# Kernel tuning notes

Measured on AMD Instinct MI355X. Metric: run time of the kernel, lower is better.

## Reference

```python
import jax, jax.numpy as jnp
import numpy as np

D_MODEL = 1024
N_HEADS = 16
D_K = D_MODEL // N_HEADS
EPS = 1e-8


def _l2_rownorm(x):
    # RowNormActivation: normalize each row (last dim) to unit L2 norm
    return x * jax.lax.rsqrt(jnp.sum(x * x, axis=-1, keepdims=True) + EPS)


def setup_inputs() -> dict:
    key = jax.random.key(0)
    ks = jax.random.split(key, 11)
    B, S = 2, 2048
    sc = 1.0 / np.sqrt(D_MODEL)
    inp = {
        "Q": jax.random.normal(ks[0], (B, S, D_MODEL), jnp.float32),
        "K": jax.random.normal(ks[1], (B, S, D_MODEL), jnp.float32),
        "V": jax.random.normal(ks[2], (B, S, D_MODEL), jnp.float32),
        "Wq_w": jax.random.normal(ks[3], (D_MODEL, D_MODEL), jnp.float32) * sc,
        "Wq_b": jnp.zeros((D_MODEL,), jnp.float32),
        "Wk_w": jax.random.normal(ks[4], (D_MODEL, D_MODEL), jnp.float32) * sc,
        "Wk_b": jnp.zeros((D_MODEL,), jnp.float32),
        "Wv_w": jax.random.normal(ks[5], (D_MODEL, D_MODEL), jnp.float32) * sc,
        "Wv_b": jnp.zeros((D_MODEL,), jnp.float32),
        "Wo_w": jax.random.normal(ks[6], (D_MODEL, D_MODEL), jnp.float32) * sc,
        "Wo_b": jnp.zeros((D_MODEL,), jnp.float32),
    }
    return inp


def reference(Q, K, V, Wq_w, Wq_b, Wk_w, Wk_b, Wv_w, Wv_b, Wo_w, Wo_b):
    B, S, _ = Q.shape
    # torch Linear: y = x @ W.T + b
    q = (Q @ Wq_w.T + Wq_b).reshape(B, S, N_HEADS, D_K).transpose(0, 2, 1, 3)
    k = (K @ Wk_w.T + Wk_b).reshape(B, S, N_HEADS, D_K).transpose(0, 2, 1, 3)
    v = (V @ Wv_w.T + Wv_b).reshape(B, S, N_HEADS, D_K).transpose(0, 2, 1, 3)
    qn = _l2_rownorm(q)
    kn = _l2_rownorm(k)
    scores = jnp.einsum("bhqd,bhkd->bhqk", qn, kn)
    attn = scores * scores  # squared similarity, no softmax (dropout=0 / eval)
    out = jnp.einsum("bhqk,bhkd->bhqd", attn, v)
    out = out.transpose(0, 2, 1, 3).reshape(B, S, D_MODEL)
    return out @ Wo_w.T + Wo_b
```

## Files before the change

kernel.cpp:

```cpp
#include <hip/hip_runtime.h>
#include <hip/hip_bf16.h>


#define D_MODEL 1024
#define N_HEADS 16
#define D_K     64
#define BATCH   2
#define SEQ     2048
#define M_TOT   (BATCH * SEQ)

typedef short  s16x8 __attribute__((ext_vector_type(8)));
typedef float  f32x4 __attribute__((ext_vector_type(4)));
typedef unsigned short ushort_t;
typedef ushort_t us4 __attribute__((ext_vector_type(4)));

__device__ __forceinline__ ushort_t f2bf(float f) {
    union { float f; unsigned int u; } x; x.f = f;
    unsigned int u = x.u;
    return (ushort_t)((u + 0x7fffu + ((u >> 16) & 1u)) >> 16);
}
__device__ __forceinline__ float bf2f(ushort_t h) {
    union { unsigned int u; float f; } x; x.u = ((unsigned int)h) << 16;
    return x.f;
}
__device__ __forceinline__ unsigned int pack2bf(float a, float b) {
    union { __hip_bfloat162 h; unsigned int u; } x;
    x.h = __float22bfloat162_rn(float2{a, b});
    return x.u;
}

__device__ __forceinline__ void gload_lds16(const ushort_t* g, ushort_t* l) {
    __builtin_amdgcn_global_load_lds(
        (__attribute__((address_space(1))) void*)(ushort_t*)g,
        (__attribute__((address_space(3))) void*)l, 16, 0, 0);
}

#define WAIT_VM(n)  asm volatile("s_waitcnt vmcnt(" #n ")" ::: "memory")
#define WAIT_LGKM0  asm volatile("s_waitcnt lgkmcnt(0)" ::: "memory")
#define BARRIER     asm volatile("s_barrier" ::: "memory")

struct ConvArgs {
    const float* src[11];
    ushort_t*    dst[11];
    int          n[11];
};

__global__ __launch_bounds__(256) void convert_kernel(ConvArgs a) {
    const int t = blockIdx.y;
    const int i = (blockIdx.x * 256 + threadIdx.x) * 4;
    if (i >= a.n[t]) return;
    const float4 v = *(const float4*)(a.src[t] + i);
    us4 p;
    p[0] = f2bf(v.x); p[1] = f2bf(v.y); p[2] = f2bf(v.z); p[3] = f2bf(v.w);
    *(us4*)(a.dst[t] + i) = p;
}

template <int BM, int MODE>
__device__ __forceinline__ void gemm_body(
    ushort_t* __restrict__ smem,
    const ushort_t* __restrict__ A,
    const ushort_t* __restrict__ W,
    const ushort_t* __restrict__ bias,
    ushort_t* __restrict__ out,
    float* __restrict__ outf,
    int bx, int by)
{
    static_assert(BM == 64 || BM == 128, "");
    constexpr int K    = 1024;
    constexpr int MF   = BM / 32;
    constexpr int BUFW = (BM + 128) * 64;
    constexpr int NIT  = K / 64;

    const int t    = threadIdx.x;
    const int wave = t >> 6;
    const int lane = t & 63;
    const int quad = lane >> 4;
    const int lc   = lane & 15;
    const int wm   = wave >> 1;
    const int wn   = wave & 1;
    const int m0   = bx * BM;
    const int n0   = by * 128;

    f32x4 acc[MF][4];
    const f32x4 zero = {0.f, 0.f, 0.f, 0.f};
#pragma unroll
    for (int i = 0; i < MF; ++i)
#pragma unroll
        for (int j = 0; j < 4; ++j) acc[i][j] = zero;

    auto stage = [&](int buf, int k0) {
        ushort_t* Ast = smem + buf * BUFW;
        ushort_t* Bst = Ast + BM * 64;
#pragma unroll
        for (int c = 0; c < MF; ++c) {
            int idx = c * 256 + t;
            int row = idx >> 3, phys = idx & 7;
            int col = (phys ^ (row & 7)) * 8;
            gload_lds16(A + (size_t)(m0 + row) * K + k0 + col, Ast + idx * 8);
        }
#pragma unroll
        for (int c = 0; c < 4; ++c) {
            int idx = c * 256 + t;
            int row = idx >> 3, phys = idx & 7;
            int col = (phys ^ (row & 7)) * 8;
            gload_lds16(W + (size_t)(n0 + row) * K + k0 + col, Bst + idx * 8);
        }
    };
    auto comp = [&](int buf) {
        ushort_t* Ast = smem + buf * BUFW;
        ushort_t* Bst = Ast + BM * 64;
#pragma unroll
        for (int ks = 0; ks < 2; ++ks) {
            const int ph = ((ks * 4 + quad) ^ (lc & 7)) * 8;
            s16x8 a[MF], b[4];
#pragma unroll
            for (int i = 0; i < MF; ++i)
                a[i] = *(const s16x8*)(Ast + (wm * (BM / 2) + i * 16 + lc) * 64 + ph);
#pragma unroll
            for (int i = 0; i < 4; ++i)
                b[i] = *(const s16x8*)(Bst + (wn * 64 + i * 16 + lc) * 64 + ph);
#pragma unroll
            for (int mf = 0; mf < MF; ++mf)
#pragma unroll
                for (int nf = 0; nf < 4; ++nf)
                    acc[mf][nf] = __builtin_amdgcn_mfma_f32_16x16x32_bf16(
                        a[mf], b[nf], acc[mf][nf], 0, 0, 0);
        }
    };

    stage(0, 0);
    stage(1, 64);
    for (int it = 0; it < NIT - 2; ++it) {
        if constexpr (BM == 128) WAIT_VM(8); else WAIT_VM(6);
        BARRIER;
        comp(it & 1);
        WAIT_LGKM0;
        BARRIER;
        stage(it & 1, (it + 2) * 64);
    }
    if constexpr (BM == 128) WAIT_VM(8); else WAIT_VM(6);
    BARRIER;
    comp((NIT - 2) & 1);
    WAIT_VM(0);
    BARRIER;
    comp((NIT - 1) & 1);

    float bv[4];
#pragma unroll
    for (int nf = 0; nf < 4; ++nf) bv[nf] = bf2f(bias[n0 + wn * 64 + nf * 16 + lc]);

    if (MODE == 0) {
#pragma unroll
        for (int mf = 0; mf < MF; ++mf)
#pragma unroll
            for (int nf = 0; nf < 4; ++nf)
#pragma unroll
                for (int r = 0; r < 4; ++r) {
                    int mg = m0 + wm * (BM / 2) + mf * 16 + quad * 4 + r;
                    int ng = n0 + wn * 64 + nf * 16 + lc;
                    outf[(size_t)mg * D_MODEL + ng] = acc[mf][nf][r] + bv[nf];
                }
    } else if (MODE == 1) {
#pragma unroll
        for (int mf = 0; mf < MF; ++mf)
#pragma unroll
            for (int r = 0; r < 4; ++r) {
                float ss = 0.f;
#pragma unroll
                for (int nf = 0; nf < 4; ++nf) {
                    float v = acc[mf][nf][r] + bv[nf];
                    acc[mf][nf][r] = v;
                    ss += v * v;
                }
                ss += __shfl_xor(ss, 1);
                ss += __shfl_xor(ss, 2);
                ss += __shfl_xor(ss, 4);
                ss += __shfl_xor(ss, 8);
                float inv = rsqrtf(ss + 1e-8f);
                int mg = m0 + wm * (BM / 2) + mf * 16 + quad * 4 + r;
                int b  = mg >> 11;
                int s  = mg & 2047;
#pragma unroll
                for (int nf = 0; nf < 4; ++nf) {
                    int ng = n0 + wn * 64 + nf * 16 + lc;
                    int h = ng >> 6, d = ng & 63;
                    out[(((size_t)(b * N_HEADS + h)) * SEQ + s) * D_K + d] =
                        f2bf(acc[mf][nf][r] * inv);
                }
            }
    } else {
        __syncthreads();
        ushort_t* vt = smem + wave * (64 * 72);
#pragma unroll
        for (int mf = 0; mf < 4; ++mf)
#pragma unroll
            for (int nf = 0; nf < 4; ++nf) {
                us4 p;
#pragma unroll
                for (int r = 0; r < 4; ++r) p[r] = f2bf(acc[mf][nf][r] + bv[nf]);
                *(us4*)(vt + (nf * 16 + lc) * 72 + mf * 16 + quad * 4) = p;
            }
        WAIT_LGKM0;
#pragma unroll
        for (int r = 0; r < 8; ++r) {
            int d  = r * 8 + (lane >> 3);
            int so = (lane & 7) * 8;
            uint4 val = *(const uint4*)(vt + d * 72 + so);
            int mg = m0 + wm * 64 + so;
            int b  = mg >> 11;
            int s  = mg & 2047;
            int ng = n0 + wn * 64 + d;
            int h = ng >> 6, dh = ng & 63;
            *(uint4*)(out + (((size_t)(b * N_HEADS + h)) * D_K + dh) * SEQ + s) = val;
        }
    }
}

__global__ __launch_bounds__(256) void qkv_kernel(
    const ushort_t* __restrict__ Qb, const ushort_t* __restrict__ Kb,
    const ushort_t* __restrict__ Vb,
    const ushort_t* __restrict__ Wq, const ushort_t* __restrict__ Wk,
    const ushort_t* __restrict__ Wv,
    const ushort_t* __restrict__ bq, const ushort_t* __restrict__ bk,
    const ushort_t* __restrict__ bv,
    ushort_t* __restrict__ qn, ushort_t* __restrict__ kn,
    ushort_t* __restrict__ vT)
{
    __shared__ __align__(16) ushort_t smem[2 * (128 + 128) * 64];
    const int z = blockIdx.z;
    if (z == 0)
        gemm_body<128, 1>(smem, Qb, Wq, bq, qn, nullptr, blockIdx.x, blockIdx.y);
    else if (z == 1)
        gemm_body<128, 1>(smem, Kb, Wk, bk, kn, nullptr, blockIdx.x, blockIdx.y);
    else
        gemm_body<128, 2>(smem, Vb, Wv, bv, vT, nullptr, blockIdx.x, blockIdx.y);
}

__global__ __launch_bounds__(256) void wo_kernel(
    const ushort_t* __restrict__ A, const ushort_t* __restrict__ W,
    const ushort_t* __restrict__ bias, float* __restrict__ outf)
{
    __shared__ __align__(16) ushort_t smem[2 * (64 + 128) * 64];
    gemm_body<64, 0>(smem, A, W, bias, nullptr, outf, blockIdx.x, blockIdx.y);
}

__global__ __launch_bounds__(256) void attn_kernel(
    const ushort_t* __restrict__ qn,
    const ushort_t* __restrict__ kn,
    const ushort_t* __restrict__ vT,
    ushort_t* __restrict__ attn_out)
{
    __shared__ __align__(16) ushort_t smem[2 * 8192];
    __shared__ __align__(16) ushort_t Pl[128 * 64];

    const int t    = threadIdx.x;
    const int wave = t >> 6;
    const int lane = t & 63;
    const int quad = lane >> 4;
    const int lc   = lane & 15;
    const int bh   = blockIdx.x;
    const int qt   = blockIdx.y;
    const int b    = bh >> 4;
    const int h    = bh & 15;

    const ushort_t* qb = qn + (size_t)bh * SEQ * D_K;
    const ushort_t* kb = kn + (size_t)bh * SEQ * D_K;
    const ushort_t* vb = vT + (size_t)bh * D_K * SEQ;
    const int q0 = qt * 128;

    s16x8 qf[8][2];
#pragma unroll
    for (int mf = 0; mf < 8; ++mf)
#pragma unroll
        for (int ks = 0; ks < 2; ++ks)
            qf[mf][ks] = *(const s16x8*)(qb + (size_t)(q0 + mf * 16 + lc) * D_K +
                                         ks * 32 + quad * 8);

    f32x4 oacc[2][4];
    const f32x4 zero = {0.f, 0.f, 0.f, 0.f};
#pragma unroll
    for (int mf = 0; mf < 2; ++mf)
#pragma unroll
        for (int df = 0; df < 4; ++df) oacc[mf][df] = zero;

    auto stage = [&](int buf, int j0) {
        ushort_t* kst = smem + buf * 8192;
        ushort_t* vst = kst + 4096;
#pragma unroll
        for (int c = 0; c < 2; ++c) {
            int idx = c * 256 + t;
            int row = idx >> 3, phys = idx & 7;
            int col = (phys ^ (row & 7)) * 8;
            gload_lds16(kb + (size_t)(j0 + row) * D_K + col, kst + idx * 8);
            gload_lds16(vb + (size_t)row * SEQ + j0 + col, vst + idx * 8);
        }
    };

    auto qk = [&](int buf) {
        ushort_t* kst = smem + buf * 8192;
        s16x8 ak[2];
#pragma unroll
        for (int ks = 0; ks < 2; ++ks)
            ak[ks] = *(const s16x8*)(kst + (wave * 16 + lc) * 64 +
                                     (((ks * 4 + quad) ^ (lc & 7)) * 8));
        const int log8 = wave * 4 + quad;
#pragma unroll
        for (int mf = 0; mf < 8; ++mf) {
            f32x4 st = zero;
#pragma unroll
            for (int ks = 0; ks < 2; ++ks)
                st = __builtin_amdgcn_mfma_f32_16x16x32_bf16(ak[ks], qf[mf][ks], st, 0, 0, 0);
            uint2 w;
            w.x = pack2bf(st[0] * st[0], st[1] * st[1]);
            w.y = pack2bf(st[2] * st[2], st[3] * st[3]);
            const int row = mf * 16 + lc;
            *(uint2*)(Pl + row * 64 + (log8 ^ lc) * 4) = w;
        }
    };

    auto pv = [&](int buf) {
        ushort_t* vst = smem + buf * 8192 + 4096;
        s16x8 bvf[4][2];
#pragma unroll
        for (int df = 0; df < 4; ++df)
#pragma unroll
            for (int ks = 0; ks < 2; ++ks)
                bvf[df][ks] = *(const s16x8*)(vst + (df * 16 + lc) * 64 +
                                              (((ks * 4 + quad) ^ (lc & 7)) * 8));
        s16x8 aa[2][2];
#pragma unroll
        for (int mfp = 0; mfp < 2; ++mfp)
#pragma unroll
            for (int ks = 0; ks < 2; ++ks) {
                const int row = wave * 32 + mfp * 16 + lc;
                const int l0  = ks * 8 + quad * 2;
                uint2 lo = *(const uint2*)(Pl + row * 64 + ((l0 ^ lc) * 4));
                uint2 hi = *(const uint2*)(Pl + row * 64 + (((l0 + 1) ^ lc) * 4));
                union { unsigned int u[4]; s16x8 v; } m;
                m.u[0] = lo.x; m.u[1] = lo.y; m.u[2] = hi.x; m.u[3] = hi.y;
                aa[mfp][ks] = m.v;
            }
#pragma unroll
        for (int mfp = 0; mfp < 2; ++mfp)
#pragma unroll
            for (int df = 0; df < 4; ++df)
#pragma unroll
                for (int ks = 0; ks < 2; ++ks)
                    oacc[mfp][df] = __builtin_amdgcn_mfma_f32_16x16x32_bf16(
                        aa[mfp][ks], bvf[df][ks], oacc[mfp][df], 0, 0, 0);
    };

    constexpr int NT = 32;
    stage(0, 0);
    stage(1, 64);
    for (int it = 0; it < NT; ++it) {
        if (it < NT - 1) { WAIT_VM(4); } else { WAIT_VM(0); }
        BARRIER;
        qk(it & 1);
        WAIT_LGKM0;
        BARRIER;
        pv(it & 1);
        if (it < NT - 2) {
            WAIT_LGKM0;
            BARRIER;
            stage(it & 1, (it + 2) * 64);
        } else if (it == NT - 2) {
            WAIT_LGKM0;
            BARRIER;
        }
    }

#pragma unroll
    for (int mfp = 0; mfp < 2; ++mfp)
#pragma unroll
        for (int df = 0; df < 4; ++df)
#pragma unroll
            for (int r = 0; r < 4; ++r) {
                int s = q0 + wave * 32 + mfp * 16 + quad * 4 + r;
                int d = df * 16 + lc;
                attn_out[((size_t)(b * SEQ + s)) * D_MODEL + h * D_K + d] =
                    f2bf(oacc[mfp][df][r]);
            }
}

extern "C" void kernel_launch(void* const* d_in, const int* in_sizes, int n_in,
                              void* d_out, int out_size, void* d_ws, size_t ws_size,
                              hipStream_t stream)
{
    const float* Qf   = (const float*)d_in[0];
    const float* Kf   = (const float*)d_in[1];
    const float* Vf   = (const float*)d_in[2];
    const float* Wqf  = (const float*)d_in[3];
    const float* Wqbf = (const float*)d_in[4];
    const float* Wkf  = (const float*)d_in[5];
    const float* Wkbf = (const float*)d_in[6];
    const float* Wvf  = (const float*)d_in[7];
    const float* Wvbf = (const float*)d_in[8];
    const float* Wof  = (const float*)d_in[9];
    const float* Wobf = (const float*)d_in[10];

    const size_t NM = (size_t)M_TOT * D_MODEL;
    const size_t NW = (size_t)D_MODEL * D_MODEL;
    const size_t NB = D_MODEL;

    ushort_t* p = (ushort_t*)d_ws;
    ushort_t* Qb  = p;  p += NM;
    ushort_t* Kb  = p;  p += NM;
    ushort_t* Vb  = p;  p += NM;
    ushort_t* Wq  = p;  p += NW;
    ushort_t* Wk  = p;  p += NW;
    ushort_t* Wv  = p;  p += NW;
    ushort_t* Wo  = p;  p += NW;
    ushort_t* bq  = p;  p += NB;
    ushort_t* bk  = p;  p += NB;
    ushort_t* bvv = p;  p += NB;
    ushort_t* bo  = p;  p += NB;
    ushort_t* qn  = p;  p += NM;
    ushort_t* kn  = p;  p += NM;
    ushort_t* vT  = p;  p += NM;
    ushort_t* ao  = p;  p += NM;

    ConvArgs ca;
    ca.src[0] = Qf;   ca.dst[0] = Qb;  ca.n[0] = (int)NM;
    ca.src[1] = Kf;   ca.dst[1] = Kb;  ca.n[1] = (int)NM;
    ca.src[2] = Vf;   ca.dst[2] = Vb;  ca.n[2] = (int)NM;
    ca.src[3] = Wqf;  ca.dst[3] = Wq;  ca.n[3] = (int)NW;
    ca.src[4] = Wkf;  ca.dst[4] = Wk;  ca.n[4] = (int)NW;
    ca.src[5] = Wvf;  ca.dst[5] = Wv;  ca.n[5] = (int)NW;
    ca.src[6] = Wof;  ca.dst[6] = Wo;  ca.n[6] = (int)NW;
    ca.src[7] = Wqbf; ca.dst[7] = bq;  ca.n[7] = (int)NB;
    ca.src[8] = Wkbf; ca.dst[8] = bk;  ca.n[8] = (int)NB;
    ca.src[9] = Wvbf; ca.dst[9] = bvv; ca.n[9] = (int)NB;
    ca.src[10] = Wobf; ca.dst[10] = bo; ca.n[10] = (int)NB;

    dim3 blk(256);
    convert_kernel<<<dim3((unsigned)(NM / (256 * 4)), 11), blk, 0, stream>>>(ca);

    qkv_kernel<<<dim3(M_TOT / 128, D_MODEL / 128, 3), blk, 0, stream>>>(
        Qb, Kb, Vb, Wq, Wk, Wv, bq, bk, bvv, qn, kn, vT);
    attn_kernel<<<dim3(BATCH * N_HEADS, SEQ / 128), blk, 0, stream>>>(qn, kn, vT, ao);
    wo_kernel<<<dim3(M_TOT / 64, D_MODEL / 128), blk, 0, stream>>>(
        ao, Wo, bo, (float*)d_out);
}
```

Before: 226.4 us.

## Shrink GEMM K-tile to 32, split attention PV over key halves, drop V transpose staging

New measurement: 253.4 us. +11.9%, slower.

```diff
diff --git a/kernel.cpp b/kernel.cpp
--- a/kernel.cpp
+++ b/kernel.cpp
@@ -66,10 +66,11 @@
     int bx, int by)
 {
     static_assert(BM == 64 || BM == 128, "");
-    constexpr int K    = 1024;
-    constexpr int MF   = BM / 32;
-    constexpr int BUFW = (BM + 128) * 64;
-    constexpr int NIT  = K / 64;
+    constexpr int K     = 1024;
+    constexpr int MF    = BM / 32;
+    constexpr int BUFW  = (BM + 128) * 32;
+    constexpr int NIT   = K / 32;
+    constexpr int APASS = (BM * 32) / 2048;
 
     const int t    = threadIdx.x;
     const int wave = t >> 6;
@@ -80,6 +81,7 @@
     const int wn   = wave & 1;
     const int m0   = bx * BM;
     const int n0   = by * 128;
+    const int flc  = (lc & 3) ^ ((lc >> 2) & 3);
 
     f32x4 acc[MF][4];
     const f32x4 zero = {0.f, 0.f, 0.f, 0.f};
@@ -90,55 +92,52 @@
 
     auto stage = [&](int buf, int k0) {
         ushort_t* Ast = smem + buf * BUFW;
-        ushort_t* Bst = Ast + BM * 64;
-#pragma unroll
-        for (int c = 0; c < MF; ++c) {
+        ushort_t* Bst = Ast + BM * 32;
+#pragma unroll
+        for (int c = 0; c < APASS; ++c) {
             int idx = c * 256 + t;
-            int row = idx >> 3, phys = idx & 7;
-            int col = (phys ^ (row & 7)) * 8;
+            int row = idx >> 2, phys = idx & 3;
+            int col = ((phys ^ ((row ^ (row >> 2)))) & 3) * 8;
             gload_lds16(A + (size_t)(m0 + row) * K + k0 + col, Ast + idx * 8);
         }
 #pragma unroll
-        for (int c = 0; c < 4; ++c) {
+        for (int c = 0; c < 2; ++c) {
             int idx = c * 256 + t;
-            int row = idx >> 3, phys = idx & 7;
-            int col = (phys ^ (row & 7)) * 8;
+            int row = idx >> 2, phys = idx & 3;
+            int col = ((phys ^ ((row ^ (row >> 2)))) & 3) * 8;
             gload_lds16(W + (size_t)(n0 + row) * K + k0 + col, Bst + idx * 8);
         }
     };
     auto comp = [&](int buf) {
         ushort_t* Ast = smem + buf * BUFW;
-        ushort_t* Bst = Ast + BM * 64;
-#pragma unroll
-        for (int ks = 0; ks < 2; ++ks) {
-            const int ph = ((ks * 4 + quad) ^ (lc & 7)) * 8;
-            s16x8 a[MF], b[4];
-#pragma unroll
-            for (int i = 0; i < MF; ++i)
-                a[i] = *(const s16x8*)(Ast + (wm * (BM / 2) + i * 16 + lc) * 64 + ph);
-#pragma unroll
-            for (int i = 0; i < 4; ++i)
-                b[i] = *(const s16x8*)(Bst + (wn * 64 + i * 16 + lc) * 64 + ph);
-#pragma unroll
-            for (int mf = 0; mf < MF; ++mf)
-#pragma unroll
-                for (int nf = 0; nf < 4; ++nf)
-                    acc[mf][nf] = __builtin_amdgcn_mfma_f32_16x16x32_bf16(
-                        a[mf], b[nf], acc[mf][nf], 0, 0, 0);
-        }
+        ushort_t* Bst = Ast + BM * 32;
+        const int ph = ((quad ^ flc) & 3) * 8;
+        s16x8 a[MF], b[4];
+#pragma unroll
+        for (int i = 0; i < MF; ++i)
+            a[i] = *(const s16x8*)(Ast + (wm * (BM / 2) + i * 16 + lc) * 32 + ph);
+#pragma unroll
+        for (int i = 0; i < 4; ++i)
+            b[i] = *(const s16x8*)(Bst + (wn * 64 + i * 16 + lc) * 32 + ph);
+#pragma unroll
+        for (int mf = 0; mf < MF; ++mf)
+#pragma unroll
+            for (int nf = 0; nf < 4; ++nf)
+                acc[mf][nf] = __builtin_amdgcn_mfma_f32_16x16x32_bf16(
+                    a[mf], b[nf], acc[mf][nf], 0, 0, 0);
     };
 
     stage(0, 0);
-    stage(1, 64);
+    stage(1, 32);
     for (int it = 0; it < NIT - 2; ++it) {
-        if constexpr (BM == 128) WAIT_VM(8); else WAIT_VM(6);
+        if constexpr (BM == 128) WAIT_VM(4); else WAIT_VM(3);
         BARRIER;
         comp(it & 1);
         WAIT_LGKM0;
         BARRIER;
-        stage(it & 1, (it + 2) * 64);
+        stage(it & 1, (it + 2) * 32);
     }
-    if constexpr (BM == 128) WAIT_VM(8); else WAIT_VM(6);
+    if constexpr (BM == 128) WAIT_VM(4); else WAIT_VM(3);
     BARRIER;
     comp((NIT - 2) & 1);
     WAIT_VM(0);
@@ -189,8 +188,6 @@
                 }
             }
     } else {
-        __syncthreads();
-        ushort_t* vt = smem + wave * (64 * 72);
 #pragma unroll
         for (int mf = 0; mf < 4; ++mf)
 #pragma unroll
@@ -198,21 +195,13 @@
                 us4 p;
 #pragma unroll
                 for (int r = 0; r < 4; ++r) p[r] = f2bf(acc[mf][nf][r] + bv[nf]);
-                *(us4*)(vt + (nf * 16 + lc) * 72 + mf * 16 + quad * 4) = p;
+                int mg = m0 + wm * 64 + mf * 16 + quad * 4;
+                int b  = mg >> 11;
+                int s  = mg & 2047;
+                int ng = n0 + wn * 64 + nf * 16 + lc;
+                int h = ng >> 6, dh = ng & 63;
+                *(us4*)(out + (((size_t)(b * N_HEADS + h)) * D_K + dh) * SEQ + s) = p;
             }
-        WAIT_LGKM0;
-#pragma unroll
-        for (int r = 0; r < 8; ++r) {
-            int d  = r * 8 + (lane >> 3);
-            int so = (lane & 7) * 8;
-            uint4 val = *(const uint4*)(vt + d * 72 + so);
-            int mg = m0 + wm * 64 + so;
-            int b  = mg >> 11;
-            int s  = mg & 2047;
-            int ng = n0 + wn * 64 + d;
-            int h = ng >> 6, dh = ng & 63;
-            *(uint4*)(out + (((size_t)(b * N_HEADS + h)) * D_K + dh) * SEQ + s) = val;
-        }
     }
 }
 
@@ -226,7 +215,7 @@
     ushort_t* __restrict__ qn, ushort_t* __restrict__ kn,
     ushort_t* __restrict__ vT)
 {
-    __shared__ __align__(16) ushort_t smem[2 * (128 + 128) * 64];
+    __shared__ __align__(16) ushort_t smem[2 * (128 + 128) * 32];
     const int z = blockIdx.z;
     if (z == 0)
         gemm_body<128, 1>(smem, Qb, Wq, bq, qn, nullptr, blockIdx.x, blockIdx.y);
@@ -240,7 +229,7 @@
     const ushort_t* __restrict__ A, const ushort_t* __restrict__ W,
     const ushort_t* __restrict__ bias, float* __restrict__ outf)
 {
-    __shared__ __align__(16) ushort_t smem[2 * (64 + 128) * 64];
+    __shared__ __align__(16) ushort_t smem[2 * (64 + 128) * 32];
     gemm_body<64, 0>(smem, A, W, bias, nullptr, outf, blockIdx.x, blockIdx.y);
 }
 
@@ -262,6 +251,8 @@
     const int qt   = blockIdx.y;
     const int b    = bh >> 4;
     const int h    = bh & 15;
+    const int qh   = wave >> 1;
+    const int jh   = wave & 1;
 
     const ushort_t* qb = qn + (size_t)bh * SEQ * D_K;
     const ushort_t* kb = kn + (size_t)bh * SEQ * D_K;
@@ -276,10 +267,10 @@
             qf[mf][ks] = *(const s16x8*)(qb + (size_t)(q0 + mf * 16 + lc) * D_K +
                                          ks * 32 + quad * 8);
 
-    f32x4 oacc[2][4];
+    f32x4 oacc[4][4];
     const f32x4 zero = {0.f, 0.f, 0.f, 0.f};
 #pragma unroll
-    for (int mf = 0; mf < 2; ++mf)
+    for (int mf = 0; mf < 4; ++mf)
 #pragma unroll
         for (int df = 0; df < 4; ++df) oacc[mf][df] = zero;
 
@@ -296,6 +287,7 @@
         }
     };
 
+    const int pwoff = (((wave * 2 + (quad >> 1)) ^ (lc & 7)) * 8) + (quad & 1) * 4;
     auto qk = [&](int buf) {
         ushort_t* kst = smem + buf * 8192;
         s16x8 ak[2];
@@ -303,7 +295,6 @@
         for (int ks = 0; ks < 2; ++ks)
             ak[ks] = *(const s16x8*)(kst + (wave * 16 + lc) * 64 +
                                      (((ks * 4 + quad) ^ (lc & 7)) * 8));
-        const int log8 = wave * 4 + quad;
 #pragma unroll
         for (int mf = 0; mf < 8; ++mf) {
             f32x4 st = zero;
@@ -313,41 +304,30 @@
             uint2 w;
             w.x = pack2bf(st[0] * st[0], st[1] * st[1]);
             w.y = pack2bf(st[2] * st[2], st[3] * st[3]);
-            const int row = mf * 16 + lc;
-            *(uint2*)(Pl + row * 64 + (log8 ^ lc) * 4) = w;
+            *(uint2*)(Pl + (mf * 16 + lc) * 64 + pwoff) = w;
         }
     };
 
     auto pv = [&](int buf) {
         ushort_t* vst = smem + buf * 8192 + 4096;
-        s16x8 bvf[4][2];
+        s16x8 bvf[4];
 #pragma unroll
         for (int df = 0; df < 4; ++df)
-#pragma unroll
-            for (int ks = 0; ks < 2; ++ks)
-                bvf[df][ks] = *(const s16x8*)(vst + (df * 16 + lc) * 64 +
-                                              (((ks * 4 + quad) ^ (lc & 7)) * 8));
-        s16x8 aa[2][2];
-#pragma unroll
-        for (int mfp = 0; mfp < 2; ++mfp)
-#pragma unroll
-            for (int ks = 0; ks < 2; ++ks) {
-                const int row = wave * 32 + mfp * 16 + lc;
-                const int l0  = ks * 8 + quad * 2;
-                uint2 lo = *(const uint2*)(Pl + row * 64 + ((l0 ^ lc) * 4));
-                uint2 hi = *(const uint2*)(Pl + row * 64 + (((l0 + 1) ^ lc) * 4));
-                union { unsigned int u[4]; s16x8 v; } m;
-                m.u[0] = lo.x; m.u[1] = lo.y; m.u[2] = hi.x; m.u[3] = hi.y;
-                aa[mfp][ks] = m.v;
-            }
-#pragma unroll
-        for (int mfp = 0; mfp < 2; ++mfp)
+            bvf[df] = *(const s16x8*)(vst + (df * 16 + lc) * 64 +
+                                      (((jh * 4 + quad) ^ (lc & 7)) * 8));
+        s16x8 aa[4];
+#pragma unroll
+        for (int mfp = 0; mfp < 4; ++mfp) {
+            const int row = qh * 64 + mfp * 16 + lc;
+            aa[mfp] = *(const s16x8*)(Pl + row * 64 +
+                                      (((jh * 4 + quad) ^ (lc & 7)) * 8));
+        }
+#pragma unroll
+        for (int mfp = 0; mfp < 4; ++mfp)
 #pragma unroll
             for (int df = 0; df < 4; ++df)
-#pragma unroll
-                for (int ks = 0; ks < 2; ++ks)
-                    oacc[mfp][df] = __builtin_amdgcn_mfma_f32_16x16x32_bf16(
-                        aa[mfp][ks], bvf[df][ks], oacc[mfp][df], 0, 0, 0);
+                oacc[mfp][df] = __builtin_amdgcn_mfma_f32_16x16x32_bf16(
+                    aa[mfp], bvf[df], oacc[mfp][df], 0, 0, 0);
     };
 
     constexpr int NT = 32;
@@ -370,17 +350,37 @@
         }
     }
 
-#pragma unroll
-    for (int mfp = 0; mfp < 2; ++mfp)
-#pragma unroll
-        for (int df = 0; df < 4; ++df)
-#pragma unroll
-            for (int r = 0; r < 4; ++r) {
-                int s = q0 + wave * 32 + mfp * 16 + quad * 4 + r;
-                int d = df * 16 + lc;
-                attn_out[((size_t)(b * SEQ + s)) * D_MODEL + h * D_K + d] =
-                    f2bf(oacc[mfp][df][r]);
-            }
+    __syncthreads();
+    float* red = (float*)smem;
+    {
+        const int reg = qh * 2 + (jh ^ 1);
+        const int dfb = (jh ^ 1) * 2;
+#pragma unroll
+        for (int mfp = 0; mfp < 4; ++mfp)
+#pragma unroll
+            for (int dd = 0; dd < 2; ++dd)
+#pragma unroll
+                for (int r = 0; r < 4; ++r)
+                    red[reg * 2048 + (mfp * 16 + quad * 4 + r) * 32 + dd * 16 + lc] =
+                        oacc[mfp][dfb + dd][r];
+    }
+    __syncthreads();
+    {
+        const int reg = qh * 2 + jh;
+        const int dfb = jh * 2;
+#pragma unroll
+        for (int mfp = 0; mfp < 4; ++mfp)
+#pragma unroll
+            for (int dd = 0; dd < 2; ++dd)
+#pragma unroll
+                for (int r = 0; r < 4; ++r) {
+                    float v = oacc[mfp][dfb + dd][r] +
+                              red[reg * 2048 + (mfp * 16 + quad * 4 + r) * 32 + dd * 16 + lc];
+                    int s = q0 + qh * 64 + mfp * 16 + quad * 4 + r;
+                    int d = (dfb + dd) * 16 + lc;
+                    attn_out[((size_t)(b * SEQ + s)) * D_MODEL + h * D_K + d] = f2bf(v);
+                }
+    }
 }
 
 extern "C" void kernel_launch(void* const* d_in, const int* in_sizes, int n_in,
```

## Software-pipeline attention loop: overlap QK of next tile with PV of previous

Applied to the files above, without the earlier changes.

New measurement: 328.5 us. +45.1%, slower.

```diff
diff --git a/kernel.cpp b/kernel.cpp
--- a/kernel.cpp
+++ b/kernel.cpp
@@ -251,7 +251,7 @@
     ushort_t* __restrict__ attn_out)
 {
     __shared__ __align__(16) ushort_t smem[2 * 8192];
-    __shared__ __align__(16) ushort_t Pl[128 * 64];
+    __shared__ __align__(16) ushort_t Pl[2 * 128 * 64];
 
     const int t    = threadIdx.x;
     const int wave = t >> 6;
@@ -283,6 +283,8 @@
 #pragma unroll
         for (int df = 0; df < 4; ++df) oacc[mf][df] = zero;
 
+    s16x8 bvr[2][4][2];
+
     auto stage = [&](int buf, int j0) {
         ushort_t* kst = smem + buf * 8192;
         ushort_t* vst = kst + 4096;
@@ -296,8 +298,9 @@
         }
     };
 
-    auto qk = [&](int buf) {
+    auto qk = [&](int buf, int pb) {
         ushort_t* kst = smem + buf * 8192;
+        ushort_t* Pb  = Pl + pb * 8192;
         s16x8 ak[2];
 #pragma unroll
         for (int ks = 0; ks < 2; ++ks)
@@ -314,19 +317,22 @@
             w.x = pack2bf(st[0] * st[0], st[1] * st[1]);
             w.y = pack2bf(st[2] * st[2], st[3] * st[3]);
             const int row = mf * 16 + lc;
-            *(uint2*)(Pl + row * 64 + (log8 ^ lc) * 4) = w;
-        }
-    };
-
-    auto pv = [&](int buf) {
+            *(uint2*)(Pb + row * 64 + (log8 ^ lc) * 4) = w;
+        }
+    };
+
+    auto load_bvf = [&](int buf, int rs) {
         ushort_t* vst = smem + buf * 8192 + 4096;
-        s16x8 bvf[4][2];
 #pragma unroll
         for (int df = 0; df < 4; ++df)
 #pragma unroll
             for (int ks = 0; ks < 2; ++ks)
-                bvf[df][ks] = *(const s16x8*)(vst + (df * 16 + lc) * 64 +
-                                              (((ks * 4 + quad) ^ (lc & 7)) * 8));
+                bvr[rs][df][ks] = *(const s16x8*)(vst + (df * 16 + lc) * 64 +
+                                                  (((ks * 4 + quad) ^ (lc & 7)) * 8));
+    };
+
+    auto pv = [&](int pb, int rs) {
+        ushort_t* Pb = Pl + pb * 8192;
         s16x8 aa[2][2];
 #pragma unroll
         for (int mfp = 0; mfp < 2; ++mfp)
@@ -334,8 +340,8 @@
             for (int ks = 0; ks < 2; ++ks) {
                 const int row = wave * 32 + mfp * 16 + lc;
                 const int l0  = ks * 8 + quad * 2;
-                uint2 lo = *(const uint2*)(Pl + row * 64 + ((l0 ^ lc) * 4));
-                uint2 hi = *(const uint2*)(Pl + row * 64 + (((l0 + 1) ^ lc) * 4));
+                uint2 lo = *(const uint2*)(Pb + row * 64 + ((l0 ^ lc) * 4));
+                uint2 hi = *(const uint2*)(Pb + row * 64 + (((l0 + 1) ^ lc) * 4));
                 union { unsigned int u[4]; s16x8 v; } m;
                 m.u[0] = lo.x; m.u[1] = lo.y; m.u[2] = hi.x; m.u[3] = hi.y;
                 aa[mfp][ks] = m.v;
@@ -347,28 +353,28 @@
 #pragma unroll
                 for (int ks = 0; ks < 2; ++ks)
                     oacc[mfp][df] = __builtin_amdgcn_mfma_f32_16x16x32_bf16(
-                        aa[mfp][ks], bvf[df][ks], oacc[mfp][df], 0, 0, 0);
+                        aa[mfp][ks], bvr[rs][df][ks], oacc[mfp][df], 0, 0, 0);
     };
 
     constexpr int NT = 32;
     stage(0, 0);
     stage(1, 64);
-    for (int it = 0; it < NT; ++it) {
-        if (it < NT - 1) { WAIT_VM(4); } else { WAIT_VM(0); }
+    WAIT_VM(4);
+    BARRIER;
+    qk(0, 0);
+    load_bvf(0, 0);
+    WAIT_LGKM0;
+    for (int it = 1; it < NT; ++it) {
+        WAIT_VM(0);
         BARRIER;
-        qk(it & 1);
+        if (it < NT - 1) stage((it + 1) & 1, (it + 1) * 64);
+        qk(it & 1, it & 1);
+        load_bvf(it & 1, it & 1);
+        pv((it - 1) & 1, (it - 1) & 1);
         WAIT_LGKM0;
-        BARRIER;
-        pv(it & 1);
-        if (it < NT - 2) {
-            WAIT_LGKM0;
-            BARRIER;
-            stage(it & 1, (it + 2) * 64);
-        } else if (it == NT - 2) {
-            WAIT_LGKM0;
-            BARRIER;
-        }
     }
+    BARRIER;
+    pv((NT - 1) & 1, (NT - 1) & 1);
 
 #pragma unroll
     for (int mfp = 0; mfp < 2; ++mfp)
```
